# Kernel tuning notes

Measured on AMD Instinct MI355X. Metric: run time of the kernel, lower is better.

The kernel has to match this reference:

```python
import jax, jax.numpy as jnp
import numpy as np

N, E, IN_DIM, H, D = 50000, 1600000, 128, 4, 32
LEAKY_ALPHA = 0.2

def _glorot(key, shape):
    r = np.sqrt(6.0 / (shape[0] + shape[1]))
    return jax.random.uniform(key, shape, jnp.float32, -r, r)

def setup_inputs() -> dict:
    key = jax.random.key(0)
    ks = jax.random.split(key, 6)
    x = jax.random.normal(ks[0], (N, IN_DIM), jnp.float32)
    edge_index = jax.random.randint(ks[1], (2, E), 0, N, jnp.int64 if jax.config.jax_enable_x64 else jnp.int32)
    W_src = _glorot(ks[2], (IN_DIM, H * D))
    W_dst = _glorot(ks[3], (IN_DIM, H * D))
    W_val = _glorot(ks[4], (IN_DIM, H * D))
    attn_vec = _glorot(ks[5], (1, H)).reshape(1, H, 1) * jnp.ones((1, H, D), jnp.float32)
    # faithful glorot for (1,H,D): fan based on shape[0]+shape[1]=1+H as in source
    r = np.sqrt(6.0 / (1 + H))
    attn_vec = jax.random.uniform(jax.random.fold_in(key, 7), (1, H, D), jnp.float32, -r, r)
    return {"x": x, "edge_index": edge_index, "W_src": W_src, "W_dst": W_dst, "W_val": W_val, "attn_vec": attn_vec}

def reference(x, edge_index, W_src, W_dst, W_val, attn_vec):
    n = x.shape[0]
    h = attn_vec.shape[1]
    d = attn_vec.shape[2]
    h_s = (x @ W_src).reshape(n, h, d)
    h_d = (x @ W_dst).reshape(n, h, d)
    h_v = (x @ W_val).reshape(n, h, d)
    src, dst = edge_index[0], edge_index[1]
    # GATv2 edge scores: a^T LeakyReLU(W_src h_i + W_dst h_j)  -> [E, H]
    middle = jax.nn.leaky_relu(h_s[src] + h_d[dst], negative_slope=LEAKY_ALPHA)
    scores = jnp.sum(middle * attn_vec, axis=-1)  # [E, H]
    # segment softmax over incoming edges of each dst node (all heads at once)
    seg_max = jax.ops.segment_max(scores, dst, num_segments=n)  # [N, H]
    exp_scores = jnp.exp(scores - seg_max[dst])
    seg_sum = jax.ops.segment_sum(exp_scores, dst, num_segments=n)
    attn = exp_scores / (seg_sum[dst] + 1e-9)  # [E, H]
    # weighted message aggregation
    messages = (attn[..., None] * h_v[src]).reshape(-1, h * d)  # [E, H*D]
    out_sum = jax.ops.segment_sum(messages, dst, num_segments=n)  # [N, H*D]
    return out_sum, attn
```

## Files before the change

### kernel.cpp

```cpp
#include <hip/hip_runtime.h>

#define LEAKY 0.2f
#define BCAP 511

typedef __attribute__((ext_vector_type(8))) short short8v;
typedef __attribute__((ext_vector_type(4))) float f32x4;
typedef _Float16 half2v __attribute__((ext_vector_type(2)));

__device__ __forceinline__ float h2f(unsigned short b) {
    union { unsigned short u; _Float16 h; } c; c.u = b; return (float)c.h;
}
__device__ __forceinline__ unsigned short f2h(float f) {
    union { unsigned short u; _Float16 h; } c; c.h = (_Float16)f; return c.u;
}
__device__ __forceinline__ half2v u2h2(unsigned u) {
    union { unsigned u; half2v h; } c; c.u = u; return c.h;
}
__device__ __forceinline__ void h4w(unsigned wx, unsigned wy, float& a, float& b, float& c, float& d) {
    a = h2f((unsigned short)(wx & 0xFFFF)); b = h2f((unsigned short)(wx >> 16));
    c = h2f((unsigned short)(wy & 0xFFFF)); d = h2f((unsigned short)(wy >> 16));
}
__device__ __forceinline__ unsigned short f2bf(float f) {
    unsigned u = __float_as_uint(f);
    return (unsigned short)((u + 0x7FFFu + ((u >> 16) & 1u)) >> 16);
}
__device__ __forceinline__ float bf2f(unsigned short b) {
    return __uint_as_float((unsigned)b << 16);
}
__device__ __forceinline__ int clampi(int v, int hi) { return v < 0 ? 0 : (v > hi ? hi : v); }
__device__ __forceinline__ int ld_idx(const int* __restrict__ ei, int is64, size_t pos) {
    return is64 ? ei[pos * 2] : ei[pos];
}
__device__ __forceinline__ half2v h2max(half2v a, half2v b) {
#if __has_builtin(__builtin_elementwise_max)
    return __builtin_elementwise_max(a, b);
#else
    half2v r; r.x = a.x > b.x ? a.x : b.x; r.y = a.y > b.y ? a.y : b.y; return r;
#endif
}
__device__ __forceinline__ half2v h2min(half2v a, half2v b) {
#if __has_builtin(__builtin_elementwise_min)
    return __builtin_elementwise_min(a, b);
#else
    half2v r; r.x = a.x < b.x ? a.x : b.x; r.y = a.y < b.y ? a.y : b.y; return r;
#endif
}
__device__ __forceinline__ float fdot2f(half2v a, half2v b, float c) {
#if __has_builtin(__builtin_amdgcn_fdot2)
    return __builtin_amdgcn_fdot2(a, b, c, false);
#else
    return (float)a.x * (float)b.x + (float)a.y * (float)b.y + c;
#endif
}

__global__ __launch_bounds__(256) void prep_kernel(
    const int* __restrict__ ei, int* __restrict__ iflag, int* __restrict__ gcursor,
    int* __restrict__ bcnt, int NB8,
    const float* __restrict__ W0, const float* __restrict__ W1, const float* __restrict__ W2,
    uint4* __restrict__ wfrag)
{
    const int b = blockIdx.x;
    if (b == 0) {
        __shared__ int nz;
        if (threadIdx.x == 0) { nz = 0; *gcursor = 0; }
        __syncthreads();
        if (ei[2 * threadIdx.x + 1] != 0) atomicOr(&nz, 1);
        __syncthreads();
        if (threadIdx.x == 0) *iflag = (nz == 0) ? 1 : 0;
    } else if (b <= 24) {
        int t = (b - 1) * 256 + threadIdx.x;
        int lane = t & 63, ks = (t >> 6) & 3, nt = (t >> 8) & 7, w = t >> 11;
        const float* W = (w == 0) ? W0 : ((w == 1) ? W1 : W2);
        int col = nt * 16 + (lane & 15);
        int k0 = ks * 32 + ((lane >> 4) & 3) * 8;
        short8v h, l;
        #pragma unroll
        for (int j = 0; j < 8; ++j) {
            float v = W[(size_t)(k0 + j) * 128 + col];
            unsigned short hb = f2bf(v);
            h[j] = (short)hb;
            l[j] = (short)f2bf(v - bf2f(hb));
        }
        size_t slot = ((size_t)nt * 4 + ks) * 64 + lane;
        *(short8v*)&wfrag[(size_t)w * 4096 + 0 * 2048 + slot] = h;
        *(short8v*)&wfrag[(size_t)w * 4096 + 1 * 2048 + slot] = l;
    } else {
        int t = (b - 25) * 256 + threadIdx.x;
        if (t < NB8) bcnt[t] = 0;
    }
}

__global__ __launch_bounds__(256) void gemm3_mfma_kernel(
    const float* __restrict__ x, const uint4* __restrict__ wfrag,
    unsigned short* __restrict__ comb_us, unsigned short* __restrict__ hdh, int N)
{
    __shared__ uint4 wsb4[4096];
    unsigned short* wsb = (unsigned short*)wsb4;
    const int tid = threadIdx.x;
    const int wave = tid >> 6;
    const int lane = tid & 63;
    const int lhi = lane >> 4;
    const int llo = lane & 15;
    const int base_row = blockIdx.x * 128 + wave * 32;

    short8v Ahi[2][4], Alo[2][4];
    #pragma unroll
    for (int rt = 0; rt < 2; ++rt) {
        #pragma unroll
        for (int ks = 0; ks < 4; ++ks) {
            int row = base_row + rt * 16 + llo;
            int rowc = row < N ? row : N - 1;
            const float* p = &x[(size_t)rowc * 128 + ks * 32 + lhi * 8];
            float4 v0 = *(const float4*)p;
            float4 v1 = *(const float4*)(p + 4);
            float vv[8] = {v0.x, v0.y, v0.z, v0.w, v1.x, v1.y, v1.z, v1.w};
            short8v h, l;
            #pragma unroll
            for (int j = 0; j < 8; ++j) {
                unsigned short hb = f2bf(vv[j]);
                h[j] = (short)hb;
                l[j] = (short)f2bf(vv[j] - bf2f(hb));
            }
            Ahi[rt][ks] = h; Alo[rt][ks] = l;
        }
    }

    for (int w = 0; w < 3; ++w) {
        __syncthreads();
        #pragma unroll
        for (int it = 0; it < 16; ++it) {
            int slot = it * 256 + tid;
            wsb4[slot] = wfrag[(size_t)w * 4096 + slot];
        }
        __syncthreads();

        f32x4 acc[2][8];
        #pragma unroll
        for (int rt = 0; rt < 2; ++rt)
            #pragma unroll
            for (int nt = 0; nt < 8; ++nt)
                acc[rt][nt] = (f32x4){0.f, 0.f, 0.f, 0.f};

        #pragma unroll
        for (int ks = 0; ks < 4; ++ks) {
            #pragma unroll
            for (int nt = 0; nt < 8; ++nt) {
                short8v Bh = *(short8v*)&wsb[((((size_t)0 * 8 + nt) * 4 + ks) * 64 + lane) * 8];
                short8v Bl = *(short8v*)&wsb[((((size_t)1 * 8 + nt) * 4 + ks) * 64 + lane) * 8];
                acc[0][nt] = __builtin_amdgcn_mfma_f32_16x16x32_bf16(Ahi[0][ks], Bh, acc[0][nt], 0, 0, 0);
                acc[1][nt] = __builtin_amdgcn_mfma_f32_16x16x32_bf16(Ahi[1][ks], Bh, acc[1][nt], 0, 0, 0);
                acc[0][nt] = __builtin_amdgcn_mfma_f32_16x16x32_bf16(Alo[0][ks], Bh, acc[0][nt], 0, 0, 0);
                acc[1][nt] = __builtin_amdgcn_mfma_f32_16x16x32_bf16(Alo[1][ks], Bh, acc[1][nt], 0, 0, 0);
                acc[0][nt] = __builtin_amdgcn_mfma_f32_16x16x32_bf16(Ahi[0][ks], Bl, acc[0][nt], 0, 0, 0);
                acc[1][nt] = __builtin_amdgcn_mfma_f32_16x16x32_bf16(Ahi[1][ks], Bl, acc[1][nt], 0, 0, 0);
            }
        }

        #pragma unroll
        for (int rt = 0; rt < 2; ++rt) {
            #pragma unroll
            for (int nt = 0; nt < 8; ++nt) {
                #pragma unroll
                for (int reg = 0; reg < 4; ++reg) {
                    int node = base_row + rt * 16 + lhi * 4 + reg;
                    int col = nt * 16 + llo;
                    if (node < N) {
                        float v = acc[rt][nt][reg];
                        if (w == 1) {
                            hdh[(size_t)node * 256 + col] = f2h(v);
                        } else {
                            int slot = (w == 2) ? 1 : 0;
                            comb_us[(size_t)node * 256 + (col >> 2) * 8 + slot * 4 + (col & 3)] = f2h(v);
                        }
                    }
                }
            }
        }
    }
}

__global__ __launch_bounds__(256) void bucket_scatter_kernel(
    const int* __restrict__ ei, const int* __restrict__ iflag,
    int* __restrict__ bcnt, uint2* __restrict__ bucket_data, int N, int E)
{
    int t = blockIdx.x * 256 + threadIdx.x;
    if (t >= E) return;
    int is64 = *iflag;
    int src = clampi(ld_idx(ei, is64, (size_t)t), N - 1);
    int dst = clampi(ld_idx(ei, is64, (size_t)E + t), N - 1);
    int slot = (dst >> 6) * 8 + (blockIdx.x & 7);
    int k = atomicAdd(&bcnt[slot], 1);
    if (k < BCAP)
        bucket_data[(size_t)slot * BCAP + k] =
            make_uint2((unsigned)src | ((unsigned)(dst & 63) << 16), (unsigned)t);
}

__global__ __launch_bounds__(256) void csr_build_kernel(
    const uint2* __restrict__ bucket_data, const int* __restrict__ bcnt,
    int* __restrict__ gcursor, int2* __restrict__ offs2,
    int2* __restrict__ sorted2, int N)
{
    __shared__ uint2 ebuf[8 * BCAP];
    __shared__ int cnt[64];
    __shared__ int pre[64];
    __shared__ int soff[9];
    __shared__ int gbase_s;
    const int b = blockIdx.x;
    const int t = threadIdx.x;
    if (t == 0) {
        int acc = 0;
        #pragma unroll
        for (int s = 0; s < 8; ++s) {
            soff[s] = acc;
            int c = bcnt[b * 8 + s];
            acc += (c < BCAP ? c : BCAP);
        }
        soff[8] = acc;
        gbase_s = atomicAdd(gcursor, acc);
    }
    if (t < 64) cnt[t] = 0;
    __syncthreads();
    const int tcnt = soff[8];
    const int gbase = gbase_s;
    #pragma unroll
    for (int s = 0; s < 8; ++s) {
        int o = soff[s], c = soff[s + 1] - o;
        const uint2* p = &bucket_data[((size_t)b * 8 + s) * BCAP];
        for (int k = t; k < c; k += 256) ebuf[o + k] = p[k];
    }
    __syncthreads();
    for (int k = t; k < tcnt; k += 256)
        atomicAdd(&cnt[(ebuf[k].x >> 16) & 63], 1);
    __syncthreads();
    if (t < 64) {
        int v = cnt[t], o = v;
        #pragma unroll
        for (int off = 1; off < 64; off <<= 1) {
            int xv = __shfl_up(v, off);
            if (t >= off) v += xv;
        }
        pre[t] = v - o;
        int node = b * 64 + t;
        if (node < N) offs2[node] = make_int2(gbase + v - o, gbase + v);
    }
    __syncthreads();
    if (t < 64) cnt[t] = pre[t];
    __syncthreads();
    for (int k = t; k < tcnt; k += 256) {
        uint2 d = ebuf[k];
        int dl = (d.x >> 16) & 63;
        int pos = gbase + atomicAdd(&cnt[dl], 1);
        sorted2[pos] = make_int2((int)(d.x & 0xFFFF), (int)d.y);
    }
}

__global__ __launch_bounds__(256) void gather_fused_kernel(
    const int2* __restrict__ offs2, const int2* __restrict__ sorted2,
    const uint4* __restrict__ comb, const unsigned short* __restrict__ hdh,
    const float* __restrict__ av,
    float* __restrict__ scores, float* __restrict__ out,
    float* __restrict__ segsum, int N)
{
    int wid = (int)(((size_t)blockIdx.x * 256 + threadIdx.x) >> 6);
    if (wid >= N) return;
    int lane = threadIdx.x & 63;
    int sub = lane >> 5;
    int le = lane & 31;
    int h = le >> 3;
    int2 be = offs2[wid];
    int beg = be.x, end = be.y;

    uint2 hw = *(const uint2*)&hdh[(size_t)wid * 256 + le * 4];
    float4 a4 = *(const float4*)&av[le * 4];
    const half2v d2_0 = u2h2(hw.x);
    const half2v d2_1 = u2h2(hw.y);
    const half2v av2_0 = {(_Float16)a4.x, (_Float16)a4.y};
    const half2v av2_1 = {(_Float16)a4.z, (_Float16)a4.w};
    const half2v hz = {(_Float16)0.f, (_Float16)0.f};

    float sum = 0.f;
    float a0 = 0.f, a1 = 0.f, a2 = 0.f, a3 = 0.f;

    int j = beg + sub;
    int2 se0 = make_int2(0, 0), se1 = make_int2(0, 0);
    uint4 c0 = make_uint4(0, 0, 0, 0);
    if (j < end)     se0 = sorted2[j];
    if (j + 2 < end) se1 = sorted2[j + 2];
    if (j < end)     c0 = comb[(size_t)se0.x * 32 + le];

    while (j < end) {
        int jn = j + 2;
        int2 se2 = make_int2(0, 0);
        uint4 c1 = make_uint4(0, 0, 0, 0);
        if (jn + 2 < end) se2 = sorted2[jn + 2];
        if (jn < end)     c1 = comb[(size_t)se1.x * 32 + le];

        half2v m0 = u2h2(c0.x) + d2_0;
        half2v m1 = u2h2(c0.y) + d2_1;
        half2v p0 = h2max(m0, hz), q0 = h2min(m0, hz);
        half2v p1 = h2max(m1, hz), q1 = h2min(m1, hz);
        float sp = fdot2f(p1, av2_1, fdot2f(p0, av2_0, 0.f));
        float sq = fdot2f(q1, av2_1, fdot2f(q0, av2_0, 0.f));
        float s = fmaf(LEAKY, sq, sp);
        s += __shfl_xor(s, 1);
        s += __shfl_xor(s, 2);
        s += __shfl_xor(s, 4);
        float w = __expf(s);
        if ((le & 7) == 0) scores[(size_t)se0.y * 4 + h] = w;
        sum += w;
        float v0, v1, v2, v3;
        h4w(c0.z, c0.w, v0, v1, v2, v3);
        a0 += w * v0; a1 += w * v1; a2 += w * v2; a3 += w * v3;

        j = jn; se0 = se1; se1 = se2; c0 = c1;
    }
    sum += __shfl_xor(sum, 32);
    a0 += __shfl_xor(a0, 32); a1 += __shfl_xor(a1, 32);
    a2 += __shfl_xor(a2, 32); a3 += __shfl_xor(a3, 32);
    float inv = 1.f / (sum + 1e-9f);
    if (sub == 0) {
        *(float4*)&out[(size_t)wid * 128 + le * 4] =
            make_float4(a0 * inv, a1 * inv, a2 * inv, a3 * inv);
        if ((le & 7) == 0) segsum[(size_t)wid * 4 + h] = inv;
    }
}

__global__ __launch_bounds__(256) void attn_write_kernel(
    const int* __restrict__ ei, const int* __restrict__ iflag,
    float* sc, const float* __restrict__ segsum, int N, int E)
{
    int t = blockIdx.x * 256 + threadIdx.x;
    if (t >= E * 4) return;
    int e = t >> 2, h = t & 3;
    int dst = clampi(ld_idx(ei, *iflag, (size_t)E + e), N - 1);
    sc[t] = sc[t] * segsum[(size_t)dst * 4 + h];
}

extern "C" void kernel_launch(void* const* d_in, const int* in_sizes, int n_in,
                              void* d_out, int out_size, void* d_ws, size_t ws_size,
                              hipStream_t stream)
{
    const float* x  = (const float*)d_in[0];
    const int* ei   = (const int*)d_in[1];
    const float* W0 = (const float*)d_in[2];
    const float* W1 = (const float*)d_in[3];
    const float* W2 = (const float*)d_in[4];
    const float* av = (const float*)d_in[5];
    const int N = in_sizes[0] / 128;
    const int E = in_sizes[1] / 2;
    const int NB = (N + 63) >> 6;

    float* out_f = (float*)d_out;
    unsigned short* hdh = (unsigned short*)out_f;
    float* out_sum = out_f;
    float* scores = out_f + (size_t)N * 128;
    uint2* bucket_data = (uint2*)scores;

    uint4* comb = (uint4*)d_ws;
    int2* sorted2 = (int2*)(comb + (size_t)N * 32);
    float* segsum = (float*)(sorted2 + (size_t)E);
    int2* offs2 = (int2*)(segsum + (size_t)N * 4);
    int* bcnt = (int*)(offs2 + N);
    int* iflag = bcnt + NB * 8;
    int* gcursor = iflag + 1;
    uint4* wfrag = (uint4*)(((uintptr_t)(gcursor + 1) + 255) & ~(uintptr_t)255);

    const int zblocks = (NB * 8 + 255) / 256;
    prep_kernel<<<25 + zblocks, 256, 0, stream>>>(
        ei, iflag, gcursor, bcnt, NB * 8, W0, W1, W2, wfrag);
    gemm3_mfma_kernel<<<(N + 127) / 128, 256, 0, stream>>>(
        x, wfrag, (unsigned short*)comb, hdh, N);
    bucket_scatter_kernel<<<(E + 255) / 256, 256, 0, stream>>>(
        ei, iflag, bcnt, bucket_data, N, E);
    csr_build_kernel<<<NB, 256, 0, stream>>>(
        bucket_data, bcnt, gcursor, offs2, sorted2, N);
    gather_fused_kernel<<<(N + 3) / 4, 256, 0, stream>>>(
        offs2, sorted2, comb, hdh, av, scores, out_sum, segsum, N);
    attn_write_kernel<<<(E * 4 + 255) / 256, 256, 0, stream>>>(
        ei, iflag, scores, segsum, N, E);
}
```

Baseline: 377.7 us.

## Merge GEMM and edge bucket scatter into one launch, halve weight LDS

Fuses the node-projection GEMM and the edge bucket-scatter into a single launch, with block ranges split by index, so the two independent stages can run concurrently and one launch is removed. The GEMM's shared weight buffer is halved by loading the hi and lo bf16 weight fragments in two phases. This improves occupancy at the cost of extra barriers and reloads. The attention rescale kernel now processes one edge per thread with float4 loads and stores instead of one head per thread.

```diff
diff --git a/kernel.cpp b/kernel.cpp
--- a/kernel.cpp
+++ b/kernel.cpp
@@ -90,12 +90,30 @@
     }
 }
 
-__global__ __launch_bounds__(256) void gemm3_mfma_kernel(
+__global__ __launch_bounds__(256) void gemm_scatter_kernel(
     const float* __restrict__ x, const uint4* __restrict__ wfrag,
-    unsigned short* __restrict__ comb_us, unsigned short* __restrict__ hdh, int N)
-{
-    __shared__ uint4 wsb4[4096];
+    unsigned short* __restrict__ comb_us, unsigned short* __restrict__ hdh,
+    const int* __restrict__ ei, const int* __restrict__ iflag,
+    int* __restrict__ bcnt, uint2* __restrict__ bucket_data,
+    int N, int E, int GB)
+{
+    __shared__ uint4 wsb4[2048];
     unsigned short* wsb = (unsigned short*)wsb4;
+
+    if ((int)blockIdx.x >= GB) {
+        int t = ((int)blockIdx.x - GB) * 256 + threadIdx.x;
+        if (t >= E) return;
+        int is64 = *iflag;
+        int src = clampi(ld_idx(ei, is64, (size_t)t), N - 1);
+        int dst = clampi(ld_idx(ei, is64, (size_t)E + t), N - 1);
+        int slot = (dst >> 6) * 8 + ((int)blockIdx.x & 7);
+        int k = atomicAdd(&bcnt[slot], 1);
+        if (k < BCAP)
+            bucket_data[(size_t)slot * BCAP + k] =
+                make_uint2((unsigned)src | ((unsigned)(dst & 63) << 16), (unsigned)t);
+        return;
+    }
+
     const int tid = threadIdx.x;
     const int wave = tid >> 6;
     const int lane = tid & 63;
@@ -128,10 +146,8 @@
     for (int w = 0; w < 3; ++w) {
         __syncthreads();
         #pragma unroll
-        for (int it = 0; it < 16; ++it) {
-            int slot = it * 256 + tid;
-            wsb4[slot] = wfrag[(size_t)w * 4096 + slot];
-        }
+        for (int it = 0; it < 8; ++it)
+            wsb4[it * 256 + tid] = wfrag[(size_t)w * 4096 + it * 256 + tid];
         __syncthreads();
 
         f32x4 acc[2][8];
@@ -145,12 +161,25 @@
         for (int ks = 0; ks < 4; ++ks) {
             #pragma unroll
             for (int nt = 0; nt < 8; ++nt) {
-                short8v Bh = *(short8v*)&wsb[((((size_t)0 * 8 + nt) * 4 + ks) * 64 + lane) * 8];
-                short8v Bl = *(short8v*)&wsb[((((size_t)1 * 8 + nt) * 4 + ks) * 64 + lane) * 8];
+                short8v Bh = *(short8v*)&wsb[(((size_t)nt * 4 + ks) * 64 + lane) * 8];
                 acc[0][nt] = __builtin_amdgcn_mfma_f32_16x16x32_bf16(Ahi[0][ks], Bh, acc[0][nt], 0, 0, 0);
                 acc[1][nt] = __builtin_amdgcn_mfma_f32_16x16x32_bf16(Ahi[1][ks], Bh, acc[1][nt], 0, 0, 0);
                 acc[0][nt] = __builtin_amdgcn_mfma_f32_16x16x32_bf16(Alo[0][ks], Bh, acc[0][nt], 0, 0, 0);
                 acc[1][nt] = __builtin_amdgcn_mfma_f32_16x16x32_bf16(Alo[1][ks], Bh, acc[1][nt], 0, 0, 0);
+            }
+        }
+
+        __syncthreads();
+        #pragma unroll
+        for (int it = 0; it < 8; ++it)
+            wsb4[it * 256 + tid] = wfrag[(size_t)w * 4096 + 2048 + it * 256 + tid];
+        __syncthreads();
+
+        #pragma unroll
+        for (int ks = 0; ks < 4; ++ks) {
+            #pragma unroll
+            for (int nt = 0; nt < 8; ++nt) {
+                short8v Bl = *(short8v*)&wsb[(((size_t)nt * 4 + ks) * 64 + lane) * 8];
                 acc[0][nt] = __builtin_amdgcn_mfma_f32_16x16x32_bf16(Ahi[0][ks], Bl, acc[0][nt], 0, 0, 0);
                 acc[1][nt] = __builtin_amdgcn_mfma_f32_16x16x32_bf16(Ahi[1][ks], Bl, acc[1][nt], 0, 0, 0);
             }
@@ -179,22 +208,6 @@
     }
 }
 
-__global__ __launch_bounds__(256) void bucket_scatter_kernel(
-    const int* __restrict__ ei, const int* __restrict__ iflag,
-    int* __restrict__ bcnt, uint2* __restrict__ bucket_data, int N, int E)
-{
-    int t = blockIdx.x * 256 + threadIdx.x;
-    if (t >= E) return;
-    int is64 = *iflag;
-    int src = clampi(ld_idx(ei, is64, (size_t)t), N - 1);
-    int dst = clampi(ld_idx(ei, is64, (size_t)E + t), N - 1);
-    int slot = (dst >> 6) * 8 + (blockIdx.x & 7);
-    int k = atomicAdd(&bcnt[slot], 1);
-    if (k < BCAP)
-        bucket_data[(size_t)slot * BCAP + k] =
-            make_uint2((unsigned)src | ((unsigned)(dst & 63) << 16), (unsigned)t);
-}
-
 __global__ __launch_bounds__(256) void csr_build_kernel(
     const uint2* __restrict__ bucket_data, const int* __restrict__ bcnt,
     int* __restrict__ gcursor, int2* __restrict__ offs2,
@@ -329,11 +342,13 @@
     const int* __restrict__ ei, const int* __restrict__ iflag,
     float* sc, const float* __restrict__ segsum, int N, int E)
 {
-    int t = blockIdx.x * 256 + threadIdx.x;
-    if (t >= E * 4) return;
-    int e = t >> 2, h = t & 3;
+    int e = blockIdx.x * 256 + threadIdx.x;
+    if (e >= E) return;
     int dst = clampi(ld_idx(ei, *iflag, (size_t)E + e), N - 1);
-    sc[t] = sc[t] * segsum[(size_t)dst * 4 + h];
+    float4 w4 = *(float4*)&sc[(size_t)e * 4];
+    float4 s4 = *(const float4*)&segsum[(size_t)dst * 4];
+    w4.x *= s4.x; w4.y *= s4.y; w4.z *= s4.z; w4.w *= s4.w;
+    *(float4*)&sc[(size_t)e * 4] = w4;
 }
 
 extern "C" void kernel_launch(void* const* d_in, const int* in_sizes, int n_in,
@@ -365,17 +380,18 @@
     int* gcursor = iflag + 1;
     uint4* wfrag = (uint4*)(((uintptr_t)(gcursor + 1) + 255) & ~(uintptr_t)255);
 
+    const int GB = (N + 127) / 128;
+    const int SB = (E + 255) / 256;
     const int zblocks = (NB * 8 + 255) / 256;
+
     prep_kernel<<<25 + zblocks, 256, 0, stream>>>(
         ei, iflag, gcursor, bcnt, NB * 8, W0, W1, W2, wfrag);
-    gemm3_mfma_kernel<<<(N + 127) / 128, 256, 0, stream>>>(
-        x, wfrag, (unsigned short*)comb, hdh, N);
-    bucket_scatter_kernel<<<(E + 255) / 256, 256, 0, stream>>>(
-        ei, iflag, bcnt, bucket_data, N, E);
+    gemm_scatter_kernel<<<GB + SB, 256, 0, stream>>>(
+        x, wfrag, (unsigned short*)comb, hdh, ei, iflag, bcnt, bucket_data, N, E, GB);
     csr_build_kernel<<<NB, 256, 0, stream>>>(
         bucket_data, bcnt, gcursor, offs2, sorted2, N);
     gather_fused_kernel<<<(N + 3) / 4, 256, 0, stream>>>(
         offs2, sorted2, comb, hdh, av, scores, out_sum, segsum, N);
-    attn_write_kernel<<<(E * 4 + 255) / 256, 256, 0, stream>>>(
+    attn_write_kernel<<<(E + 255) / 256, 256, 0, stream>>>(
         ei, iflag, scores, segsum, N, E);
 }
```

New measurement: 360.9 us. 4.5% less time.
